# Kernel optimization log

Hardware: AMD Instinct MI355X
Metric: run time of the kernel (lower is better)

The kernel has to match this reference:

```python
import jax, jax.numpy as jnp
import numpy as np

N_FFT = 2048
HOP = 512
PAD = N_FFT // 2  # 1024, center padding
FREQ_BINS = N_FFT // 2 + 1  # 1025


def _fourier_kernels():
    # freq_scale='no', window='hann' (fftbins=True): w[n] = 0.5 - 0.5*cos(2*pi*n/N)
    s = np.arange(N_FFT, dtype=np.float64)
    win = 0.5 - 0.5 * np.cos(2.0 * np.pi * s / N_FFT)
    k = np.arange(FREQ_BINS, dtype=np.float64)[:, None]
    phase = 2.0 * np.pi * k * s[None, :] / N_FFT  # (freq_bins, n_fft)
    wsin = (win[None, :] * np.sin(phase)).astype(np.float32)
    wcos = (win[None, :] * np.cos(phase)).astype(np.float32)
    return wcos, wsin


def setup_inputs() -> dict:
    key = jax.random.key(0)
    x = jax.random.normal(key, (32, 220500), dtype=jnp.float32)
    wcos, wsin = _fourier_kernels()
    return {"x": x, "wcos": jnp.asarray(wcos), "wsin": jnp.asarray(wsin)}


def reference(x, wcos, wsin):
    # x: (B, L). center=True, pad_mode='reflect'
    xp = jnp.pad(x, ((0, 0), (PAD, PAD)), mode="reflect")[:, None, :]  # (B,1,Lp)
    dn = ("NCH", "OIH", "NCH")
    # one conv with both bases stacked -> (B, 2*freq_bins, T)
    kern = jnp.concatenate([wcos, wsin], axis=0)[:, None, :]  # (2F,1,n_fft)
    spec = jax.lax.conv_general_dilated(
        xp, kern, window_strides=(HOP,), padding="VALID", dimension_numbers=dn
    )
    real, imag = spec[:, :FREQ_BINS, :], spec[:, FREQ_BINS:, :]
    # output_format='Complex': stack (real, -imag) on last axis
    return jnp.stack([real, -imag], axis=-1)  # (B, F, T, 2)
```

## Files before the change

kernel.cpp:

```cpp
#include <hip/hip_runtime.h>
#include <hip/hip_bf16.h>

#define L_IN   220500
#define PADK   1024
#define LP     222548
#define LPP    222560
#define BATCH  32
#define HOPSZ  512
#define T_FR   431
#define F_BINS 1025
#define M_TOT  (BATCH * T_FR)
#define N_GEMM 2048
#define K_TOT  2048
#define NT_K   32
#define GEMM_BLOCKS 432
#define NYQ_BLOCKS  48
#define XBLOCKS 3488
#define WBLOCKS 2048

typedef short short8 __attribute__((ext_vector_type(8)));
typedef float floatx4 __attribute__((ext_vector_type(4)));

__device__ __forceinline__ void glds16(const void* g, void* l) {
    __builtin_amdgcn_global_load_lds(
        (const __attribute__((address_space(1))) void*)g,
        (__attribute__((address_space(3))) void*)l, 16, 0, 0);
}

__device__ __forceinline__ short f2bf(float f) {
    __hip_bfloat16 h = __float2bfloat16(f);
    return *reinterpret_cast<short*>(&h);
}

__global__ void k_prep(const float* __restrict__ x,
                       const float* __restrict__ wcos, const float* __restrict__ wsin,
                       __hip_bfloat16* __restrict__ xp, __hip_bfloat16* __restrict__ wb) {
    int blk = blockIdx.x;
    if (blk < XBLOCKS) {
        int b = blk / 109, ix = blk - b * 109;
        int i0 = (ix * 256 + threadIdx.x) * 8;
        if (i0 >= LP) return;
        const float* xb = x + (size_t)b * L_IN;
        __hip_bfloat16* xpb = xp + (size_t)b * LPP;
        if (i0 >= PADK && i0 + 8 <= PADK + L_IN) {
            const float4* s4 = (const float4*)(xb + (i0 - PADK));
            float4 a = s4[0], d = s4[1];
            short8 o;
            o[0]=f2bf(a.x); o[1]=f2bf(a.y); o[2]=f2bf(a.z); o[3]=f2bf(a.w);
            o[4]=f2bf(d.x); o[5]=f2bf(d.y); o[6]=f2bf(d.z); o[7]=f2bf(d.w);
            *(short8*)((short*)xpb + i0) = o;
        } else {
            for (int u = 0; u < 8; ++u) {
                int i = i0 + u;
                if (i >= LP) break;
                int j = i - PADK;
                if (j < 0) j = -j;
                if (j >= L_IN) j = 2 * L_IN - 2 - j;
                xpb[i] = __float2bfloat16(xb[j]);
            }
        }
    } else {
        int i0 = ((blk - XBLOCKS) * 256 + threadIdx.x) * 8;
        int np = i0 >> 11;
        int k  = i0 & (K_TOT - 1);
        int kf = np >> 1;
        const float* src = ((np & 1) ? wsin : wcos) + (size_t)kf * K_TOT + k;
        float4 a = ((const float4*)src)[0], d = ((const float4*)src)[1];
        short8 o;
        o[0]=f2bf(a.x); o[1]=f2bf(a.y); o[2]=f2bf(a.z); o[3]=f2bf(a.w);
        o[4]=f2bf(d.x); o[5]=f2bf(d.y); o[6]=f2bf(d.z); o[7]=f2bf(d.w);
        *(short8*)((short*)wb + i0) = o;
    }
}

#define BARRIER { asm volatile("" ::: "memory"); __builtin_amdgcn_s_barrier(); asm volatile("" ::: "memory"); }
#define VMW(N)  asm volatile("s_waitcnt vmcnt(" #N ")" ::: "memory")
#define SCHED0  __builtin_amdgcn_sched_barrier(0)
#define SP1     __builtin_amdgcn_s_setprio(1)
#define SP0     __builtin_amdgcn_s_setprio(0)

__global__ __launch_bounds__(512, 2) void k_gemm(
    const __hip_bfloat16* __restrict__ xp,
    const __hip_bfloat16* __restrict__ wb,
    const float* __restrict__ wcos,
    float* __restrict__ out) {

    __shared__ short lds[65536];

    const int tid   = threadIdx.x;
    const int wave  = tid >> 6;
    const int lane  = tid & 63;

    if (blockIdx.x >= GEMM_BLOCKS) {
        const int gw = (blockIdx.x - GEMM_BLOCKS) * 8 + wave;
        const float* wr = wcos + (size_t)1024 * K_TOT;
        for (int f = gw; f < M_TOT; f += NYQ_BLOCKS * 8) {
            int b = f / T_FR, t = f - b * T_FR;
            const __hip_bfloat16* xr = xp + (size_t)b * LPP + t * HOPSZ;
            float sum = 0.f;
            #pragma unroll
            for (int i = 0; i < 4; ++i) {
                int s = i * 512 + lane * 8;
                short8 xv = *(const short8*)((const short*)xr + s);
                const float4* wv = (const float4*)(wr + s);
                float4 w0 = wv[0], w1 = wv[1];
                float xs[8];
                #pragma unroll
                for (int u = 0; u < 8; ++u)
                    xs[u] = __uint_as_float(((unsigned)(unsigned short)xv[u]) << 16);
                sum += xs[0]*w0.x + xs[1]*w0.y + xs[2]*w0.z + xs[3]*w0.w
                     + xs[4]*w1.x + xs[5]*w1.y + xs[6]*w1.z + xs[7]*w1.w;
            }
            #pragma unroll
            for (int off = 32; off > 0; off >>= 1) sum += __shfl_xor(sum, off);
            if (lane == 0) {
                float2 v; v.x = sum; v.y = 0.f;
                ((float2*)out)[((size_t)b * F_BINS + 1024) * T_FR + t] = v;
            }
        }
        return;
    }

    const int quad  = lane >> 4;
    const int l15   = lane & 15;
    const int waveM = wave >> 2;
    const int waveN = wave & 3;

    const int bn = blockIdx.x & 7;
    const int bm = blockIdx.x >> 3;

    int arow[2][2], brow[2][2];
    #pragma unroll
    for (int h = 0; h < 2; ++h)
        #pragma unroll
        for (int q = 0; q < 2; ++q) {
            int m = bm * 256 + h * 128 + wave * 16 + q * 8 + (lane >> 3);
            if (m > M_TOT - 1) m = M_TOT - 1;
            int b = m / T_FR, t = m - b * T_FR;
            arow[h][q] = b * LPP + t * HOPSZ;
            int n = bn * 256 + h * 128 + wave * 16 + q * 8 + (lane >> 3);
            brow[h][q] = n * K_TOT;
        }
    const int colo = (((lane & 7) ^ (lane >> 3)) << 3);

#define STA(BUF,H,K0) { _Pragma("unroll") for (int q = 0; q < 2; ++q) \
        glds16(xp + arow[H][q] + (K0) + colo, &lds[((BUF)<<14) + ((H)<<13) + (wave*16 + q*8)*64]); }
#define STB(BUF,H,K0) { _Pragma("unroll") for (int q = 0; q < 2; ++q) \
        glds16(wb + brow[H][q] + (K0) + colo, &lds[32768 + ((BUF)<<14) + ((H)<<13) + (wave*16 + q*8)*64]); }
#define RDA(BUF,H) { _Pragma("unroll") for (int jm = 0; jm < 4; ++jm) { \
        int R = waveM*64 + jm*16 + l15; \
        _Pragma("unroll") for (int ks = 0; ks < 2; ++ks) \
            xf[jm][ks] = *(const short8*)&lds[((BUF)<<14) + ((H)<<13) + R*64 + (((ks*4+quad) ^ (R & 7)) << 3)]; } }
#define RDB(BUF,H,WF) { _Pragma("unroll") for (int jn = 0; jn < 2; ++jn) { \
        int R = waveN*32 + jn*16 + l15; \
        _Pragma("unroll") for (int ks = 0; ks < 2; ++ks) \
            WF[jn][ks] = *(const short8*)&lds[32768 + ((BUF)<<14) + ((H)<<13) + R*64 + (((ks*4+quad) ^ (R & 7)) << 3)]; } }
#define MFMA16(ACC, WF) { _Pragma("unroll") for (int jm = 0; jm < 4; ++jm) \
        _Pragma("unroll") for (int jn = 0; jn < 2; ++jn) \
        _Pragma("unroll") for (int ks = 0; ks < 2; ++ks) \
            ACC[jm][jn] = __builtin_amdgcn_mfma_f32_16x16x32_bf16(WF[jn][ks], xf[jm][ks], ACC[jm][jn], 0, 0, 0); }

    short8 xf[4][2], wf0[2][2], wf1[2][2];
    floatx4 a00[4][2] = {}, a01[4][2] = {}, a10[4][2] = {}, a11[4][2] = {};

    STA(0,0,0); STB(0,0,0); STB(0,1,0); STA(0,1,0);
    STA(1,0,64); STB(1,0,64); STB(1,1,64);
    VMW(6);
    BARRIER;
    RDA(0,0); RDB(0,0,wf0);

#define TILE(T, BUF) { \
     \
    RDB(BUF, 1, wf1); \
    if ((T) + 1 < NT_K) STA(BUF^1, 1, ((T)+1)*64); \
    SCHED0; \
    SP1; MFMA16(a00, wf0); SP0; \
    BARRIER; \
     \
    if ((T) + 2 < NT_K) STA(BUF, 0, ((T)+2)*64); \
    SCHED0; \
    SP1; MFMA16(a01, wf1); SP0; \
    RDA(BUF, 1); \
    BARRIER; \
     \
    if ((T) + 2 < NT_K) STB(BUF, 0, ((T)+2)*64); \
    SCHED0; \
    SP1; MFMA16(a10, wf0); SP0; \
    if ((T) + 1 < NT_K) { if ((T) < NT_K - 2) { VMW(8); } else { VMW(4); } } \
    BARRIER; \
     \
    if ((T) + 1 < NT_K) RDB(BUF^1, 0, wf0); \
    if ((T) + 2 < NT_K) STB(BUF, 1, ((T)+2)*64); \
    SCHED0; \
    SP1; MFMA16(a11, wf1); SP0; \
    if ((T) + 1 < NT_K) RDA(BUF^1, 0); \
    if ((T) == NT_K - 2) { VMW(0); } else if ((T) < NT_K - 2) { VMW(6); } \
    if ((T) + 1 < NT_K) BARRIER; \
}

    #pragma unroll 1
    for (int T = 0; T < NT_K; T += 2) {
        TILE(T, 0);
        TILE(T + 1, 1);
    }

    float2* __restrict__ out2 = (float2*)out;
#define EPI(ACC, QM, QN) { _Pragma("unroll") for (int jm = 0; jm < 4; ++jm) { \
        int m = bm*256 + QM*128 + waveM*64 + jm*16 + l15; \
        if (m < M_TOT) { \
            int b = m / T_FR, t = m - b * T_FR; \
            long tbase = (long)b * (F_BINS * T_FR) + t; \
            _Pragma("unroll") for (int jn = 0; jn < 2; ++jn) { \
                int nb = bn*256 + QN*128 + waveN*32 + jn*16 + quad*4; \
                _Pragma("unroll") for (int p = 0; p < 2; ++p) { \
                    int k = (nb + 2*p) >> 1; \
                    float2 v; v.x = ACC[jm][jn][2*p]; v.y = -ACC[jm][jn][2*p+1]; \
                    out2[tbase + (long)k * T_FR] = v; \
                } } } } }
    EPI(a00, 0, 0); EPI(a01, 0, 1); EPI(a10, 1, 0); EPI(a11, 1, 1);
}

extern "C" void kernel_launch(void* const* d_in, const int* in_sizes, int n_in,
                              void* d_out, int out_size, void* d_ws, size_t ws_size,
                              hipStream_t stream) {
    const float* x    = (const float*)d_in[0];
    const float* wcos = (const float*)d_in[1];
    const float* wsin = (const float*)d_in[2];
    float* out = (float*)d_out;

    __hip_bfloat16* xp = (__hip_bfloat16*)d_ws;
    __hip_bfloat16* wb = (__hip_bfloat16*)((char*)d_ws + (size_t)BATCH * LPP * sizeof(__hip_bfloat16));

    k_prep<<<XBLOCKS + WBLOCKS, 256, 0, stream>>>(x, wcos, wsin, xp, wb);
    k_gemm<<<GEMM_BLOCKS + NYQ_BLOCKS, 512, 0, stream>>>(xp, wb, wcos, out);
}
```

Before: 259.6 us.

## Shrink GEMM tile to 128x256 with triple-buffered K32 stages

Replaces the 256x256 block tile, 64-wide K steps and the hand-interleaved four-quadrant schedule with a 128x256 tile, 32-wide K steps and a three-stage rotating LDS buffer. Each wave now owns a 64x64 accumulator block. LDS use drops from 128KB to 72KB and launch bounds rise to four blocks per CU. This doubles the block count to improve occupancy and CU balance, at the cost of lower data reuse per block and more barriers per unit of work.

After: 274.3 us. +5.7%, slower.

```diff
diff --git a/kernel.cpp b/kernel.cpp
--- a/kernel.cpp
+++ b/kernel.cpp
@@ -12,8 +12,8 @@
 #define M_TOT  (BATCH * T_FR)
 #define N_GEMM 2048
 #define K_TOT  2048
-#define NT_K   32
-#define GEMM_BLOCKS 432
+#define NT_K   64
+#define GEMM_BLOCKS 864
 #define NYQ_BLOCKS  48
 #define XBLOCKS 3488
 #define WBLOCKS 2048
@@ -79,17 +79,17 @@
 #define SP1     __builtin_amdgcn_s_setprio(1)
 #define SP0     __builtin_amdgcn_s_setprio(0)
 
-__global__ __launch_bounds__(512, 2) void k_gemm(
+__global__ __launch_bounds__(512, 4) void k_gemm(
     const __hip_bfloat16* __restrict__ xp,
     const __hip_bfloat16* __restrict__ wb,
     const float* __restrict__ wcos,
     float* __restrict__ out) {
 
-    __shared__ short lds[65536];
-
-    const int tid   = threadIdx.x;
-    const int wave  = tid >> 6;
-    const int lane  = tid & 63;
+    __shared__ short lds[36864];
+
+    const int tid  = threadIdx.x;
+    const int wave = tid >> 6;
+    const int lane = tid & 63;
 
     if (blockIdx.x >= GEMM_BLOCKS) {
         const int gw = (blockIdx.x - GEMM_BLOCKS) * 8 + wave;
@@ -129,95 +129,78 @@
     const int bn = blockIdx.x & 7;
     const int bm = blockIdx.x >> 3;
 
-    int arow[2][2], brow[2][2];
+    const int l4 = lane >> 2, lc = lane & 3;
+    const int swz = (lc ^ (l4 & 3)) * 8;
+    int am = bm * 128 + wave * 16 + l4;
+    if (am > M_TOT - 1) am = M_TOT - 1;
+    const int ab_ = am / T_FR, at_ = am - ab_ * T_FR;
+    const int aoff  = ab_ * LPP + at_ * HOPSZ + swz;
+    const int bnrow = bn * 256 + wave * 32 + l4;
+    const int boff0 = bnrow * K_TOT + swz;
+    const int boff1 = (bnrow + 16) * K_TOT + swz;
+    const int adst  = wave * 512;
+    const int bdst  = wave * 1024;
+
+    const int rchunk = (quad ^ (l15 & 3)) * 8;
+    const int ara = (waveM * 64 + l15) * 32 + rchunk;
+    const int bra = (waveN * 64 + l15) * 32 + rchunk;
+
+#define STAGE(BUF, K0) { \
+        glds16(xp + aoff  + (K0), &lds[(BUF) * 4096 + adst]); \
+        glds16(wb + boff0 + (K0), &lds[12288 + (BUF) * 8192 + bdst]); \
+        glds16(wb + boff1 + (K0), &lds[12288 + (BUF) * 8192 + bdst + 512]); }
+#define READS(BUF) { \
+        _Pragma("unroll") for (int i = 0; i < 4; ++i) \
+            wf[i] = *(const short8*)&lds[12288 + (BUF) * 8192 + bra + i * 512]; \
+        _Pragma("unroll") for (int j = 0; j < 4; ++j) \
+            xf[j] = *(const short8*)&lds[(BUF) * 4096 + ara + j * 512]; }
+
+    short8 xf[4], wf[4];
+    floatx4 acc[4][4] = {};
+
+    STAGE(0, 0);
+    STAGE(1, 32);
+    VMW(3);
+    BARRIER;
+
+    int r0 = 0, r1 = 1, r2 = 2;
+    #pragma unroll 1
+    for (int t = 0; t < NT_K; ++t) {
+        if (t < NT_K - 2) STAGE(r2, (t + 2) * 32);
+        SCHED0;
+        READS(r0);
+        SP1;
+        #pragma unroll
+        for (int i = 0; i < 4; ++i)
+            #pragma unroll
+            for (int j = 0; j < 4; ++j)
+                acc[i][j] = __builtin_amdgcn_mfma_f32_16x16x32_bf16(wf[i], xf[j], acc[i][j], 0, 0, 0);
+        SP0;
+        if (t < NT_K - 1) {
+            if (t < NT_K - 2) { VMW(3); } else { VMW(0); }
+            BARRIER;
+        }
+        int tmp = r0; r0 = r1; r1 = r2; r2 = tmp;
+    }
+
+    float2* __restrict__ out2 = (float2*)out;
     #pragma unroll
-    for (int h = 0; h < 2; ++h)
+    for (int j = 0; j < 4; ++j) {
+        int m = bm * 128 + waveM * 64 + j * 16 + l15;
+        if (m >= M_TOT) continue;
+        int b = m / T_FR, t = m - b * T_FR;
+        long tbase = (long)b * (F_BINS * T_FR) + t;
         #pragma unroll
-        for (int q = 0; q < 2; ++q) {
-            int m = bm * 256 + h * 128 + wave * 16 + q * 8 + (lane >> 3);
-            if (m > M_TOT - 1) m = M_TOT - 1;
-            int b = m / T_FR, t = m - b * T_FR;
-            arow[h][q] = b * LPP + t * HOPSZ;
-            int n = bn * 256 + h * 128 + wave * 16 + q * 8 + (lane >> 3);
-            brow[h][q] = n * K_TOT;
-        }
-    const int colo = (((lane & 7) ^ (lane >> 3)) << 3);
-
-#define STA(BUF,H,K0) { _Pragma("unroll") for (int q = 0; q < 2; ++q) \
-        glds16(xp + arow[H][q] + (K0) + colo, &lds[((BUF)<<14) + ((H)<<13) + (wave*16 + q*8)*64]); }
-#define STB(BUF,H,K0) { _Pragma("unroll") for (int q = 0; q < 2; ++q) \
-        glds16(wb + brow[H][q] + (K0) + colo, &lds[32768 + ((BUF)<<14) + ((H)<<13) + (wave*16 + q*8)*64]); }
-#define RDA(BUF,H) { _Pragma("unroll") for (int jm = 0; jm < 4; ++jm) { \
-        int R = waveM*64 + jm*16 + l15; \
-        _Pragma("unroll") for (int ks = 0; ks < 2; ++ks) \
-            xf[jm][ks] = *(const short8*)&lds[((BUF)<<14) + ((H)<<13) + R*64 + (((ks*4+quad) ^ (R & 7)) << 3)]; } }
-#define RDB(BUF,H,WF) { _Pragma("unroll") for (int jn = 0; jn < 2; ++jn) { \
-        int R = waveN*32 + jn*16 + l15; \
-        _Pragma("unroll") for (int ks = 0; ks < 2; ++ks) \
-            WF[jn][ks] = *(const short8*)&lds[32768 + ((BUF)<<14) + ((H)<<13) + R*64 + (((ks*4+quad) ^ (R & 7)) << 3)]; } }
-#define MFMA16(ACC, WF) { _Pragma("unroll") for (int jm = 0; jm < 4; ++jm) \
-        _Pragma("unroll") for (int jn = 0; jn < 2; ++jn) \
-        _Pragma("unroll") for (int ks = 0; ks < 2; ++ks) \
-            ACC[jm][jn] = __builtin_amdgcn_mfma_f32_16x16x32_bf16(WF[jn][ks], xf[jm][ks], ACC[jm][jn], 0, 0, 0); }
-
-    short8 xf[4][2], wf0[2][2], wf1[2][2];
-    floatx4 a00[4][2] = {}, a01[4][2] = {}, a10[4][2] = {}, a11[4][2] = {};
-
-    STA(0,0,0); STB(0,0,0); STB(0,1,0); STA(0,1,0);
-    STA(1,0,64); STB(1,0,64); STB(1,1,64);
-    VMW(6);
-    BARRIER;
-    RDA(0,0); RDB(0,0,wf0);
-
-#define TILE(T, BUF) { \
-     \
-    RDB(BUF, 1, wf1); \
-    if ((T) + 1 < NT_K) STA(BUF^1, 1, ((T)+1)*64); \
-    SCHED0; \
-    SP1; MFMA16(a00, wf0); SP0; \
-    BARRIER; \
-     \
-    if ((T) + 2 < NT_K) STA(BUF, 0, ((T)+2)*64); \
-    SCHED0; \
-    SP1; MFMA16(a01, wf1); SP0; \
-    RDA(BUF, 1); \
-    BARRIER; \
-     \
-    if ((T) + 2 < NT_K) STB(BUF, 0, ((T)+2)*64); \
-    SCHED0; \
-    SP1; MFMA16(a10, wf0); SP0; \
-    if ((T) + 1 < NT_K) { if ((T) < NT_K - 2) { VMW(8); } else { VMW(4); } } \
-    BARRIER; \
-     \
-    if ((T) + 1 < NT_K) RDB(BUF^1, 0, wf0); \
-    if ((T) + 2 < NT_K) STB(BUF, 1, ((T)+2)*64); \
-    SCHED0; \
-    SP1; MFMA16(a11, wf1); SP0; \
-    if ((T) + 1 < NT_K) RDA(BUF^1, 0); \
-    if ((T) == NT_K - 2) { VMW(0); } else if ((T) < NT_K - 2) { VMW(6); } \
-    if ((T) + 1 < NT_K) BARRIER; \
-}
-
-    #pragma unroll 1
-    for (int T = 0; T < NT_K; T += 2) {
-        TILE(T, 0);
-        TILE(T + 1, 1);
-    }
-
-    float2* __restrict__ out2 = (float2*)out;
-#define EPI(ACC, QM, QN) { _Pragma("unroll") for (int jm = 0; jm < 4; ++jm) { \
-        int m = bm*256 + QM*128 + waveM*64 + jm*16 + l15; \
-        if (m < M_TOT) { \
-            int b = m / T_FR, t = m - b * T_FR; \
-            long tbase = (long)b * (F_BINS * T_FR) + t; \
-            _Pragma("unroll") for (int jn = 0; jn < 2; ++jn) { \
-                int nb = bn*256 + QN*128 + waveN*32 + jn*16 + quad*4; \
-                _Pragma("unroll") for (int p = 0; p < 2; ++p) { \
-                    int k = (nb + 2*p) >> 1; \
-                    float2 v; v.x = ACC[jm][jn][2*p]; v.y = -ACC[jm][jn][2*p+1]; \
-                    out2[tbase + (long)k * T_FR] = v; \
-                } } } } }
-    EPI(a00, 0, 0); EPI(a01, 0, 1); EPI(a10, 1, 0); EPI(a11, 1, 1);
+        for (int i = 0; i < 4; ++i) {
+            int nb = bn * 256 + waveN * 64 + i * 16 + quad * 4;
+            #pragma unroll
+            for (int p = 0; p < 2; ++p) {
+                int k = (nb + 2 * p) >> 1;
+                float2 v; v.x = acc[i][j][2 * p]; v.y = -acc[i][j][2 * p + 1];
+                out2[tbase + (long)k * T_FR] = v;
+            }
+        }
+    }
 }
 
 extern "C" void kernel_launch(void* const* d_in, const int* in_sizes, int n_in,
```
